# Kernel optimization log

Measured on AMD Instinct MI355X. Metric: run time of the kernel, lower is better.

Reference implementation:

```python
import jax, jax.numpy as jnp
import numpy as np

E, N, F = 50000, 25000, 32

def setup_inputs() -> dict:
    key = jax.random.key(0)
    ks = jax.random.split(key, 8)
    efeat = jax.random.normal(ks[0], (E, F), dtype=jnp.float32) * 0.2
    initial_efeats = jax.random.normal(ks[1], (E, F), dtype=jnp.float32) * 0.2
    # msg_fn / attn_fn: Linear(F, F*F)
    Wm = jax.random.normal(ks[2], (F * F, F), dtype=jnp.float32) * 0.05
    bm = jnp.zeros((F * F,), dtype=jnp.float32)
    Wa = jax.random.normal(ks[3], (F * F, F), dtype=jnp.float32) * 0.05
    ba = jnp.zeros((F * F,), dtype=jnp.float32)
    src = jax.random.randint(ks[4], (E,), 0, N, dtype=jnp.int32)
    dst = jax.random.randint(ks[5], (E,), 0, N, dtype=jnp.int32)
    return {"efeat": efeat, "initial_efeats": initial_efeats, "Wm": Wm, "bm": bm,
            "Wa": Wa, "ba": ba, "src": src, "dst": dst, "num_nodes": N}

def reference(efeat, initial_efeats, Wm, bm, Wa, ba, src, dst, num_nodes):
    e, f = efeat.shape
    # edge-conditioned transform matrices: [E, F, F]
    w_m = (efeat @ Wm.T + bm).reshape(e, f, f)
    w_a = (efeat @ Wa.T + ba).reshape(e, f, f)
    h = efeat[:, :, None]                 # [E, F, 1]
    ih = initial_efeats[:, :, None]       # [E, F, 1]
    e1 = w_m * h                          # [E, F, F]
    exp_e2 = jnp.exp(w_a * h)             # [E, F, F]
    initial_e1 = w_m * ih
    exp_initial_e2 = jnp.exp(w_a * ih)
    # scatter-sum exp weights to destination nodes, gather back at src
    sum_exp_node = jax.ops.segment_sum(exp_e2, dst, num_segments=num_nodes)  # [N, F, F]
    sum_exp = sum_exp_node[src] - exp_e2 + exp_initial_e2
    h1 = exp_e2 * e1
    initial_h1 = exp_initial_e2 * initial_e1
    m_node = jax.ops.segment_sum(h1, dst, num_segments=num_nodes)            # [N, F, F]
    h2 = (m_node[src] - h1 + initial_h1) / sum_exp
    return h2.sum(axis=1)                 # [E, F]
```

## Files before the change

### kernel.cpp

```cpp
#include <hip/hip_runtime.h>
#include <hip/hip_fp16.h>
#include <math.h>
#include <stdint.h>


#define FDIM   32
#define NNODES 25000
#define NPB    8

typedef __attribute__((ext_vector_type(8))) short bf16x8;
typedef __attribute__((ext_vector_type(4))) float f32x4;

__device__ __forceinline__ unsigned short f2bf(float f) {
    unsigned u = __float_as_uint(f);
    return (unsigned short)((u + 0x7FFFu + ((u >> 16) & 1u)) >> 16);
}
__device__ __forceinline__ unsigned f2e5(float f) {
    unsigned short hb = __half_as_ushort(__float2half(f));
    return (unsigned)((unsigned short)((hb + 0x7Fu + ((hb >> 8) & 1u)) >> 8)) & 0xFFu;
}
__device__ __forceinline__ void dec2(unsigned p, float& am, float& aa) {
    am = __half2float(__ushort_as_half((unsigned short)(p << 8)));
    aa = __half2float(__ushort_as_half((unsigned short)(p & 0xFF00u)));
}

__global__ __launch_bounds__(256) void zero_f4(float4* __restrict__ p, int n4) {
    int i = blockIdx.x * blockDim.x + threadIdx.x;
    int stride = gridDim.x * blockDim.x;
    float4 z = make_float4(0.f, 0.f, 0.f, 0.f);
    for (; i < n4; i += stride) p[i] = z;
}

__global__ __launch_bounds__(256) void k_hist(
    const int* __restrict__ src, const int* __restrict__ dst,
    int* __restrict__ cnt_src, int* __restrict__ cnt_dst, int E) {
    int e = blockIdx.x * blockDim.x + threadIdx.x;
    if (e < E) {
        atomicAdd(&cnt_dst[dst[e]], 1);
        atomicAdd(&cnt_src[src[e]], 1);
    }
}

__global__ __launch_bounds__(256) void k_scan2_prep(
    const int* __restrict__ cnt_dst, int* __restrict__ off_dst, int* __restrict__ cur_dst,
    const int* __restrict__ cnt_src, int* __restrict__ off_src, int* __restrict__ cur_src,
    int n,
    const float* __restrict__ Wm, const float* __restrict__ Wa,
    short* __restrict__ wbuf)
{
    if (blockIdx.x >= 2) {
        int idx = (blockIdx.x - 2) * blockDim.x + threadIdx.x;
        if (idx >= 2 * 64 * 64) return;
        int mat  = idx >> 12;
        int jt   = (idx >> 6) & 63;
        int lane = idx & 63;
        const float* W = mat ? Wa : Wm;
        const float* s = W + (size_t)(jt * 16 + (lane & 15)) * FDIM + (lane >> 4) * 8;
        bf16x8 v;
#pragma unroll
        for (int t = 0; t < 8; ++t) v[t] = (short)f2bf(s[t]);
        *(bf16x8*)(wbuf + (size_t)idx * 8) = v;
        return;
    }
    const int* cnt = blockIdx.x ? cnt_src : cnt_dst;
    int* off = blockIdx.x ? off_src : off_dst;
    int* cur = blockIdx.x ? cur_src : cur_dst;
    __shared__ int wsum[4];
    __shared__ int carry_sh;
    const int tid = threadIdx.x, lane = tid & 63, w = tid >> 6;
    if (tid == 0) carry_sh = 0;
    __syncthreads();
    for (int base = 0; base < n; base += 1024) {
        int i0 = base + tid * 4;
        int v0 = (i0 + 0 < n) ? cnt[i0 + 0] : 0;
        int v1 = (i0 + 1 < n) ? cnt[i0 + 1] : 0;
        int v2 = (i0 + 2 < n) ? cnt[i0 + 2] : 0;
        int v3 = (i0 + 3 < n) ? cnt[i0 + 3] : 0;
        int s = v0 + v1 + v2 + v3;
        int inc = s;
        for (int d = 1; d < 64; d <<= 1) {
            int t = __shfl_up(inc, d, 64);
            if (lane >= d) inc += t;
        }
        if (lane == 63) wsum[w] = inc;
        __syncthreads();
        int wbase = 0;
        for (int k = 0; k < w; ++k) wbase += wsum[k];
        int carry = carry_sh;
        int excl = carry + wbase + inc - s;
        if (i0 + 0 < n) { off[i0 + 0] = excl; cur[i0 + 0] = excl; } excl += v0;
        if (i0 + 1 < n) { off[i0 + 1] = excl; cur[i0 + 1] = excl; } excl += v1;
        if (i0 + 2 < n) { off[i0 + 2] = excl; cur[i0 + 2] = excl; } excl += v2;
        if (i0 + 3 < n) { off[i0 + 3] = excl; cur[i0 + 3] = excl; }
        __syncthreads();
        if (tid == 255) carry_sh = carry + wbase + inc;
    }
    __syncthreads();
    if (tid == 0) off[n] = carry_sh;
}

__global__ __launch_bounds__(256) void k_scatter(
    const int* __restrict__ src, const int* __restrict__ dst,
    int* __restrict__ cur_src, int* __restrict__ cur_dst,
    int* __restrict__ eb_src, int* __restrict__ eb_dst, int E) {
    int e = blockIdx.x * blockDim.x + threadIdx.x;
    if (e < E) {
        int p = atomicAdd(&cur_dst[dst[e]], 1); eb_dst[p] = e;
        int q = atomicAdd(&cur_src[src[e]], 1); eb_src[q] = e;
    }
}

__global__ __launch_bounds__(256) void gemm(
    const float* __restrict__ efeat,
    const float* __restrict__ bm, const float* __restrict__ ba,
    const short* __restrict__ wbuf,
    unsigned short* __restrict__ buf, int E)
{
    const int lane = threadIdx.x & 63;
    const int wid  = threadIdx.x >> 6;
    const int et   = blockIdx.x * 4 + wid;
    if (et * 16 >= E) return;
    const int r16 = lane & 15;
    const int kq  = lane >> 4;

    const float* xa = efeat + (size_t)(et * 16 + r16) * FDIM + kq * 8;
    bf16x8 afrag;
#pragma unroll
    for (int t = 0; t < 8; ++t) afrag[t] = (short)f2bf(xa[t]);

    for (int jt = 0; jt < 64; ++jt) {
        bf16x8 bfm = *(const bf16x8*)(wbuf + ((size_t)(jt)      * 64 + lane) * 8);
        bf16x8 bfa = *(const bf16x8*)(wbuf + ((size_t)(64 + jt) * 64 + lane) * 8);
        const int j = jt * 16 + r16;
        const float biasm = bm[j], biasa = ba[j];
        f32x4 accm = {biasm, biasm, biasm, biasm};
        f32x4 acca = {biasa, biasa, biasa, biasa};
        accm = __builtin_amdgcn_mfma_f32_16x16x32_bf16(afrag, bfm, accm, 0, 0, 0);
        acca = __builtin_amdgcn_mfma_f32_16x16x32_bf16(afrag, bfa, acca, 0, 0, 0);
#pragma unroll
        for (int r = 0; r < 4; ++r) {
            int e = et * 16 + kq * 4 + r;
            unsigned pk = f2e5(accm[r]) | (f2e5(acca[r]) << 8);
            buf[(size_t)e * 1024 + j] = (unsigned short)pk;
        }
    }
}

__global__ __launch_bounds__(256) void consume(
    const float* __restrict__ efeat, const float* __restrict__ ifeat,
    const unsigned short* __restrict__ buf,
    const int* __restrict__ off_dst, const int* __restrict__ eb_dst,
    const int* __restrict__ off_src, const int* __restrict__ eb_src,
    float* __restrict__ out)
{
    __shared__ float red[2][4][8][4];
    const int tid = threadIdx.x;
    const int iidx = tid >> 3;
    const int wv  = tid >> 6;
    const int lb  = tid & 63;
    int par = 0;

    const int n0 = blockIdx.x * NPB;
    const int n1 = min(NNODES, n0 + NPB);
    for (int n = n0; n < n1; ++n) {
        float S[4] = {0.f, 0.f, 0.f, 0.f};
        float M[4] = {0.f, 0.f, 0.f, 0.f};
        const int a0 = off_dst[n], a1 = off_dst[n + 1];
        for (int idx = a0; idx < a1; ++idx) {
            int e = __builtin_amdgcn_readfirstlane(eb_dst[idx]);
            uint2 pv = *(const uint2*)(buf + (size_t)e * 1024 + 4 * tid);
            float xi = efeat[e * FDIM + iidx];
            unsigned pq[4] = {pv.x & 0xFFFFu, pv.x >> 16,
                              pv.y & 0xFFFFu, pv.y >> 16};
#pragma unroll
            for (int q = 0; q < 4; ++q) {
                float am, aa; dec2(pq[q], am, aa);
                float e2 = __expf(aa * xi);
                S[q] += e2;
                M[q] = fmaf(e2, am * xi, M[q]);
            }
        }
        const int b0 = off_src[n], b1 = off_src[n + 1];
        for (int idx = b0; idx < b1; ++idx) {
            int e = __builtin_amdgcn_readfirstlane(eb_src[idx]);
            uint2 pv = *(const uint2*)(buf + (size_t)e * 1024 + 4 * tid);
            float xi  = efeat[e * FDIM + iidx];
            float x0i = ifeat[e * FDIM + iidx];
            unsigned pq[4] = {pv.x & 0xFFFFu, pv.x >> 16,
                              pv.y & 0xFFFFu, pv.y >> 16};
            float acc[4];
#pragma unroll
            for (int q = 0; q < 4; ++q) {
                float am, aa; dec2(pq[q], am, aa);
                float e2  = __expf(aa * xi);
                float h1  = e2 * (am * xi);
                float ei2 = __expf(aa * x0i);
                float ih1 = ei2 * (am * x0i);
                float den = (S[q] - e2) + ei2;
                float num = (M[q] - h1) + ih1;
                float h2  = num * __builtin_amdgcn_rcpf(den);
                if (!isfinite(h2)) h2 = 0.f;
                acc[q] = h2;
            }
#pragma unroll
            for (int q = 0; q < 4; ++q) {
                acc[q] += __shfl_xor(acc[q], 8, 64);
                acc[q] += __shfl_xor(acc[q], 16, 64);
                acc[q] += __shfl_xor(acc[q], 32, 64);
            }
            if (lb < 8)
                *(float4*)&red[par][wv][lb][0] =
                    make_float4(acc[0], acc[1], acc[2], acc[3]);
            __syncthreads();
            if (tid < 32) {
                int bb = tid >> 2, q = tid & 3;
                float s = red[par][0][bb][q] + red[par][1][bb][q]
                        + red[par][2][bb][q] + red[par][3][bb][q];
                out[(size_t)e * FDIM + tid] = s;
            }
            par ^= 1;
        }
    }
}

extern "C" void kernel_launch(void* const* d_in, const int* in_sizes, int n_in,
                              void* d_out, int out_size, void* d_ws, size_t ws_size,
                              hipStream_t stream) {
    const float* efeat = (const float*)d_in[0];
    const float* ifeat = (const float*)d_in[1];
    const float* Wm    = (const float*)d_in[2];
    const float* bm    = (const float*)d_in[3];
    const float* Wa    = (const float*)d_in[4];
    const float* ba    = (const float*)d_in[5];
    const int*   src   = (const int*)d_in[6];
    const int*   dst   = (const int*)d_in[7];
    const int E = in_sizes[6];
    const int N = NNODES;
    float* out = (float*)d_out;

    int* cnt_dst = (int*)d_ws;
    int* cnt_src = cnt_dst + N;
    int* off_dst = cnt_src + N;
    int* off_src = off_dst + (N + 1);
    int* cur_dst = off_src + (N + 1);
    int* cur_src = cur_dst + N;
    int* eb_dst  = cur_src + N;
    int* eb_src  = eb_dst + E;
    short* wbuf  = (short*)(((uintptr_t)(eb_src + E) + 255) & ~(uintptr_t)255);
    unsigned short* buf =
        (unsigned short*)(((uintptr_t)(wbuf + 2 * 64 * 64 * 8) + 255) & ~(uintptr_t)255);

    zero_f4<<<64, 256, 0, stream>>>((float4*)cnt_dst, (2 * N) / 4);
    k_hist<<<(E + 255) / 256, 256, 0, stream>>>(src, dst, cnt_src, cnt_dst, E);
    k_scan2_prep<<<34, 256, 0, stream>>>(cnt_dst, off_dst, cur_dst,
                                         cnt_src, off_src, cur_src, N,
                                         Wm, Wa, wbuf);
    k_scatter<<<(E + 255) / 256, 256, 0, stream>>>(src, dst, cur_src, cur_dst,
                                                   eb_src, eb_dst, E);

    const int etiles = (E + 15) / 16;
    gemm<<<(etiles + 3) / 4, 256, 0, stream>>>(efeat, bm, ba, wbuf, buf, E);
    consume<<<(N + NPB - 1) / NPB, 256, 0, stream>>>(efeat, ifeat, buf,
                                                     off_dst, eb_dst,
                                                     off_src, eb_src, out);
}
```

Measured before the change: 224.8 us.

## Map one wavefront per node in consume and pack fp8 via cvt_pkrtz

The consume kernel changes from one 256-thread block serially walking 8 nodes to one wavefront per node. Each lane now holds 16 matrix entries and reads them with 16-byte vector loads. The per-edge output reduction uses only wave shuffles, which removes the LDS staging and the __syncthreads per source edge. In the gemm, fp8-e5 packing now uses a packed round-toward-zero half conversion plus a byte permute instead of manual round-to-nearest. That changes rounding slightly and raises register pressure per lane in consume.

```diff
diff --git a/kernel.cpp b/kernel.cpp
--- a/kernel.cpp
+++ b/kernel.cpp
@@ -6,22 +6,24 @@
 
 #define FDIM   32
 #define NNODES 25000
-#define NPB    8
 
 typedef __attribute__((ext_vector_type(8))) short bf16x8;
 typedef __attribute__((ext_vector_type(4))) float f32x4;
+typedef __attribute__((ext_vector_type(8))) unsigned short us8;
 
 __device__ __forceinline__ unsigned short f2bf(float f) {
     unsigned u = __float_as_uint(f);
     return (unsigned short)((u + 0x7FFFu + ((u >> 16) & 1u)) >> 16);
 }
-__device__ __forceinline__ unsigned f2e5(float f) {
-    unsigned short hb = __half_as_ushort(__float2half(f));
-    return (unsigned)((unsigned short)((hb + 0x7Fu + ((hb >> 8) & 1u)) >> 8)) & 0xFFu;
-}
-__device__ __forceinline__ void dec2(unsigned p, float& am, float& aa) {
-    am = __half2float(__ushort_as_half((unsigned short)(p << 8)));
-    aa = __half2float(__ushort_as_half((unsigned short)(p & 0xFF00u)));
+__device__ __forceinline__ unsigned short pack_e5(float am, float aa) {
+    auto hp = __builtin_amdgcn_cvt_pkrtz(am, aa);
+    unsigned u;
+    __builtin_memcpy(&u, &hp, 4);
+    return (unsigned short)__builtin_amdgcn_perm(0u, u, 0x0301u);
+}
+__device__ __forceinline__ void dec2(unsigned v, float& am, float& aa) {
+    am = __half2float(__ushort_as_half((unsigned short)((v & 0xFFu) << 8)));
+    aa = __half2float(__ushort_as_half((unsigned short)(v & 0xFF00u)));
 }
 
 __global__ __launch_bounds__(256) void zero_f4(float4* __restrict__ p, int n4) {
@@ -140,8 +142,7 @@
 #pragma unroll
         for (int r = 0; r < 4; ++r) {
             int e = et * 16 + kq * 4 + r;
-            unsigned pk = f2e5(accm[r]) | (f2e5(acca[r]) << 8);
-            buf[(size_t)e * 1024 + j] = (unsigned short)pk;
+            buf[(size_t)e * 1024 + j] = pack_e5(accm[r], acca[r]);
         }
     }
 }
@@ -153,72 +154,69 @@
     const int* __restrict__ off_src, const int* __restrict__ eb_src,
     float* __restrict__ out)
 {
-    __shared__ float red[2][4][8][4];
-    const int tid = threadIdx.x;
-    const int iidx = tid >> 3;
-    const int wv  = tid >> 6;
-    const int lb  = tid & 63;
-    int par = 0;
-
-    const int n0 = blockIdx.x * NPB;
-    const int n1 = min(NNODES, n0 + NPB);
-    for (int n = n0; n < n1; ++n) {
-        float S[4] = {0.f, 0.f, 0.f, 0.f};
-        float M[4] = {0.f, 0.f, 0.f, 0.f};
-        const int a0 = off_dst[n], a1 = off_dst[n + 1];
-        for (int idx = a0; idx < a1; ++idx) {
-            int e = __builtin_amdgcn_readfirstlane(eb_dst[idx]);
-            uint2 pv = *(const uint2*)(buf + (size_t)e * 1024 + 4 * tid);
-            float xi = efeat[e * FDIM + iidx];
-            unsigned pq[4] = {pv.x & 0xFFFFu, pv.x >> 16,
-                              pv.y & 0xFFFFu, pv.y >> 16};
-#pragma unroll
-            for (int q = 0; q < 4; ++q) {
-                float am, aa; dec2(pq[q], am, aa);
+    const int l  = threadIdx.x & 63;
+    const int w  = threadIdx.x >> 6;
+    const int n  = blockIdx.x * 4 + w;
+    if (n >= NNODES) return;
+    const int ih = l >> 2;
+
+    float S[16], M[16];
+#pragma unroll
+    for (int t = 0; t < 16; ++t) { S[t] = 0.f; M[t] = 0.f; }
+
+    const int a0 = off_dst[n], a1 = off_dst[n + 1];
+    for (int idx = a0; idx < a1; ++idx) {
+        int e = __builtin_amdgcn_readfirstlane(eb_dst[idx]);
+#pragma unroll
+        for (int qq = 0; qq < 2; ++qq) {
+            us8 pv = *(const us8*)(buf + (size_t)e * 1024 + qq * 512 + l * 8);
+            float xi = efeat[e * FDIM + qq * 16 + ih];
+#pragma unroll
+            for (int t = 0; t < 8; ++t) {
+                float am, aa; dec2(pv[t], am, aa);
                 float e2 = __expf(aa * xi);
-                S[q] += e2;
-                M[q] = fmaf(e2, am * xi, M[q]);
+                S[qq * 8 + t] += e2;
+                M[qq * 8 + t] = fmaf(e2, am * xi, M[qq * 8 + t]);
             }
         }
-        const int b0 = off_src[n], b1 = off_src[n + 1];
-        for (int idx = b0; idx < b1; ++idx) {
-            int e = __builtin_amdgcn_readfirstlane(eb_src[idx]);
-            uint2 pv = *(const uint2*)(buf + (size_t)e * 1024 + 4 * tid);
-            float xi  = efeat[e * FDIM + iidx];
-            float x0i = ifeat[e * FDIM + iidx];
-            unsigned pq[4] = {pv.x & 0xFFFFu, pv.x >> 16,
-                              pv.y & 0xFFFFu, pv.y >> 16};
-            float acc[4];
-#pragma unroll
-            for (int q = 0; q < 4; ++q) {
-                float am, aa; dec2(pq[q], am, aa);
+    }
+
+    const int b0 = off_src[n], b1 = off_src[n + 1];
+    for (int idx = b0; idx < b1; ++idx) {
+        int e = __builtin_amdgcn_readfirstlane(eb_src[idx]);
+        float acc[8];
+#pragma unroll
+        for (int t = 0; t < 8; ++t) acc[t] = 0.f;
+#pragma unroll
+        for (int qq = 0; qq < 2; ++qq) {
+            us8 pv = *(const us8*)(buf + (size_t)e * 1024 + qq * 512 + l * 8);
+            float xi  = efeat[e * FDIM + qq * 16 + ih];
+            float x0i = ifeat[e * FDIM + qq * 16 + ih];
+#pragma unroll
+            for (int t = 0; t < 8; ++t) {
+                float am, aa; dec2(pv[t], am, aa);
                 float e2  = __expf(aa * xi);
                 float h1  = e2 * (am * xi);
                 float ei2 = __expf(aa * x0i);
                 float ih1 = ei2 * (am * x0i);
-                float den = (S[q] - e2) + ei2;
-                float num = (M[q] - h1) + ih1;
+                float den = (S[qq * 8 + t] - e2) + ei2;
+                float num = (M[qq * 8 + t] - h1) + ih1;
                 float h2  = num * __builtin_amdgcn_rcpf(den);
                 if (!isfinite(h2)) h2 = 0.f;
-                acc[q] = h2;
+                acc[t] += h2;
             }
-#pragma unroll
-            for (int q = 0; q < 4; ++q) {
-                acc[q] += __shfl_xor(acc[q], 8, 64);
-                acc[q] += __shfl_xor(acc[q], 16, 64);
-                acc[q] += __shfl_xor(acc[q], 32, 64);
-            }
-            if (lb < 8)
-                *(float4*)&red[par][wv][lb][0] =
-                    make_float4(acc[0], acc[1], acc[2], acc[3]);
-            __syncthreads();
-            if (tid < 32) {
-                int bb = tid >> 2, q = tid & 3;
-                float s = red[par][0][bb][q] + red[par][1][bb][q]
-                        + red[par][2][bb][q] + red[par][3][bb][q];
-                out[(size_t)e * FDIM + tid] = s;
-            }
-            par ^= 1;
+        }
+#pragma unroll
+        for (int t = 0; t < 8; ++t) {
+            acc[t] += __shfl_xor(acc[t], 4, 64);
+            acc[t] += __shfl_xor(acc[t], 8, 64);
+            acc[t] += __shfl_xor(acc[t], 16, 64);
+            acc[t] += __shfl_xor(acc[t], 32, 64);
+        }
+        if (l < 4) {
+            float* op = out + (size_t)e * FDIM + l * 8;
+            *(float4*)op       = make_float4(acc[0], acc[1], acc[2], acc[3]);
+            *(float4*)(op + 4) = make_float4(acc[4], acc[5], acc[6], acc[7]);
         }
     }
 }
@@ -260,7 +258,7 @@
 
     const int etiles = (E + 15) / 16;
     gemm<<<(etiles + 3) / 4, 256, 0, stream>>>(efeat, bm, ba, wbuf, buf, E);
-    consume<<<(N + NPB - 1) / NPB, 256, 0, stream>>>(efeat, ifeat, buf,
-                                                     off_dst, eb_dst,
-                                                     off_src, eb_src, out);
-}
+    consume<<<(N + 3) / 4, 256, 0, stream>>>(efeat, ifeat, buf,
+                                             off_dst, eb_dst,
+                                             off_src, eb_src, out);
+}
```

Result: no change. 222.1 us (-1.2%).
